# Kernel tuning notes

Hardware: AMD Instinct MI355X
Metric: run time of the kernel (lower is better)

The kernel has to match this reference:

```python
import jax, jax.numpy as jnp
import numpy as np

E_NODES_C = 50000   # constraints
E_NODES_V = 100000  # variables
N_EDGES = 1600000
EMB = 64
EDGE_NFEATS = 1
N_LAYERS = 2
N_CONVS = 2 * N_LAYERS  # v_to_c and c_to_v per layer
EPS = 1e-5


def setup_inputs() -> dict:
    key = jax.random.key(0)
    ks = jax.random.split(key, 24)
    s = 1.0 / np.sqrt(EMB)
    inp = {
        "constraint_features": jax.random.normal(ks[0], (E_NODES_C, EMB), jnp.float32),
        "variable_features": jax.random.normal(ks[1], (E_NODES_V, EMB), jnp.float32),
        "edge_indices": jnp.stack([
            jax.random.randint(ks[2], (N_EDGES,), 0, E_NODES_C, jnp.int32),
            jax.random.randint(ks[3], (N_EDGES,), 0, E_NODES_V, jnp.int32),
        ]),
        "edge_features": jax.random.normal(ks[4], (N_EDGES, EDGE_NFEATS), jnp.float32),
        # stacked params for the 4 conv blocks
        "Wl": jax.random.normal(ks[5], (N_CONVS, EMB, EMB), jnp.float32) * s,
        "bl": jnp.zeros((N_CONVS, EMB), jnp.float32),
        "We": jax.random.normal(ks[6], (N_CONVS, EMB, EDGE_NFEATS), jnp.float32) * s,
        "Wr": jax.random.normal(ks[7], (N_CONVS, EMB, EMB), jnp.float32) * s,
        "g1": jnp.ones((N_CONVS, EMB), jnp.float32),
        "b1": jnp.zeros((N_CONVS, EMB), jnp.float32),
        "Wf": jax.random.normal(ks[8], (N_CONVS, EMB, EMB), jnp.float32) * s,
        "bf": jnp.zeros((N_CONVS, EMB), jnp.float32),
        "g2": jnp.ones((N_CONVS, EMB), jnp.float32),
        "b2": jnp.zeros((N_CONVS, EMB), jnp.float32),
        "Wo1": jax.random.normal(ks[9], (N_CONVS, EMB, 2 * EMB), jnp.float32) * s,
        "bo1": jnp.zeros((N_CONVS, EMB), jnp.float32),
        "Wo2": jax.random.normal(ks[10], (N_CONVS, EMB, EMB), jnp.float32) * s,
        "bo2": jnp.zeros((N_CONVS, EMB), jnp.float32),
    }
    return inp


def _layer_norm(x, g, b):
    m = jnp.mean(x, axis=-1, keepdims=True)
    v = jnp.mean(jnp.square(x - m), axis=-1, keepdims=True)
    return (x - m) * jax.lax.rsqrt(v + EPS) * g + b


def _conv(k, left, src, dst, ef, right, P):
    # message: Lin(right_i) + Lin_nobias(edge) + Lin_nobias(left_j)
    h = (right[dst] @ P["Wl"][k].T + P["bl"][k]
         + ef @ P["We"][k].T
         + left[src] @ P["Wr"][k].T)                       # [E, emb]
    h = jax.nn.relu(_layer_norm(h, P["g1"][k], P["b1"][k]))
    h = h @ P["Wf"][k].T + P["bf"][k]
    agg = jax.ops.segment_sum(h, dst, num_segments=right.shape[0])  # [N_right, emb]
    z = jnp.concatenate([_layer_norm(agg, P["g2"][k], P["b2"][k]), right], axis=-1)
    return jax.nn.relu(z @ P["Wo1"][k].T + P["bo1"][k]) @ P["Wo2"][k].T + P["bo2"][k]


def reference(constraint_features, variable_features, edge_indices, edge_features,
              Wl, bl, We, Wr, g1, b1, Wf, bf, g2, b2, Wo1, bo1, Wo2, bo2):
    P = dict(Wl=Wl, bl=bl, We=We, Wr=Wr, g1=g1, b1=b1, Wf=Wf, bf=bf,
             g2=g2, b2=b2, Wo1=Wo1, bo1=bo1, Wo2=Wo2, bo2=bo2)
    ci, vi = edge_indices[0], edge_indices[1]
    c, v = constraint_features, variable_features
    for i in range(N_LAYERS):
        # v_to_c: left=variables (src=vi), right=constraints (dst=ci)
        c = c + _conv(2 * i, v, vi, ci, edge_features, c, P)
        # c_to_v: left=constraints (src=ci), right=variables (dst=vi)
        v = v + _conv(2 * i + 1, c, ci, vi, edge_features, v, P)
    return (c, v)
```

## Files before the change

kernel.cpp:

```cpp
#include <hip/hip_runtime.h>

#define EMB   64
#define NCON  50000
#define NVAR  100000
#define NEDGE 1600000
#define EPSLN 1e-5f

#define PADEC (NEDGE + 15 * NCON)
#define PADEV (NEDGE + 15 * NVAR)

#define HCHUNK 12544
#define HSEG   32
#define HCHC   4
#define HCHV   8

typedef _Float16 half2_t __attribute__((ext_vector_type(2)));
typedef _Float16 f16x8  __attribute__((ext_vector_type(8)));
typedef float    f32x2  __attribute__((ext_vector_type(2)));
typedef float    f32x4  __attribute__((ext_vector_type(4)));

template <int CTRL, int RMASK>
__device__ __forceinline__ float dpp_add_f(float x) {
    int m = __builtin_amdgcn_update_dpp(0, __builtin_bit_cast(int, x), CTRL, RMASK, 0xf, true);
    return x + __builtin_bit_cast(float, m);
}
__device__ __forceinline__ float wtotal64(float x) {
    x = dpp_add_f<0x111, 0xf>(x);
    x = dpp_add_f<0x112, 0xf>(x);
    x = dpp_add_f<0x114, 0xf>(x);
    x = dpp_add_f<0x118, 0xf>(x);
    x = dpp_add_f<0x142, 0xa>(x);
    x = dpp_add_f<0x143, 0xc>(x);
    return __builtin_bit_cast(float, __builtin_amdgcn_readlane(__builtin_bit_cast(int, x), 63));
}
template <int CTRL, int RMASK>
__device__ __forceinline__ int dpp_add_i(int x) {
    return x + __builtin_amdgcn_update_dpp(0, x, CTRL, RMASK, 0xf, true);
}
__device__ __forceinline__ int wtotal64_i(int x) {
    x = dpp_add_i<0x111, 0xf>(x);
    x = dpp_add_i<0x112, 0xf>(x);
    x = dpp_add_i<0x114, 0xf>(x);
    x = dpp_add_i<0x118, 0xf>(x);
    x = dpp_add_i<0x142, 0xa>(x);
    x = dpp_add_i<0x143, 0xc>(x);
    return __builtin_amdgcn_readlane(x, 63);
}

__device__ __forceinline__ float dot2f(half2_t a, half2_t b, float c) {
    return __builtin_amdgcn_fdot2(a, b, c, false);
}

__device__ __forceinline__ half2_t hmax2(half2_t a, half2_t b) {
#if defined(__has_builtin) && __has_builtin(__builtin_elementwise_max)
    return __builtin_elementwise_max(a, b);
#else
    half2_t r;
    r.x = a.x > b.x ? a.x : b.x;
    r.y = a.y > b.y ? a.y : b.y;
    return r;
#endif
}

__device__ __forceinline__ float matvec_f16(const _Float16* __restrict__ buf,
                                            const half2_t* __restrict__ wh, float acc) {
    const float4* hp4 = (const float4*)buf;
    float a0 = acc, a1 = 0.0f, a2 = 0.0f, a3 = 0.0f;
#pragma unroll
    for (int j4 = 0; j4 < 8; ++j4) {
        float4 t = hp4[j4];
        a0 = dot2f(wh[4 * j4 + 0], __builtin_bit_cast(half2_t, t.x), a0);
        a1 = dot2f(wh[4 * j4 + 1], __builtin_bit_cast(half2_t, t.y), a1);
        a2 = dot2f(wh[4 * j4 + 2], __builtin_bit_cast(half2_t, t.z), a2);
        a3 = dot2f(wh[4 * j4 + 3], __builtin_bit_cast(half2_t, t.w), a3);
    }
    return (a0 + a1) + (a2 + a3);
}

__device__ __forceinline__ void load_w_f16(const float* __restrict__ W, int stride,
                                           int lane, half2_t* wh) {
#pragma unroll
    for (int j4 = 0; j4 < 16; ++j4) {
        float4 t = *(const float4*)(W + (size_t)lane * stride + j4 * 4);
        wh[2 * j4 + 0] = half2_t{(_Float16)t.x, (_Float16)t.y};
        wh[2 * j4 + 1] = half2_t{(_Float16)t.z, (_Float16)t.w};
    }
}

__device__ __forceinline__ f16x8 cvt8_f16(float4 u, float4 v) {
    f16x8 r;
    r[0] = (_Float16)u.x; r[1] = (_Float16)u.y; r[2] = (_Float16)u.z; r[3] = (_Float16)u.w;
    r[4] = (_Float16)v.x; r[5] = (_Float16)v.y; r[6] = (_Float16)v.z; r[7] = (_Float16)v.w;
    return r;
}


__global__ __launch_bounds__(256) void hist_part_kernel(
        const int* __restrict__ ci, const int* __restrict__ vi,
        int* __restrict__ partC, int* __restrict__ partV, int E) {
    __shared__ int lh[HCHUNK];
    const int seg  = blockIdx.x % HSEG;
    const int cg   = blockIdx.x / HSEG;
    const bool isC = cg < HCHC;
    const int chunk = isC ? cg : cg - HCHC;
    const int base  = chunk * HCHUNK;
    const int* __restrict__ dst = isC ? ci : vi;
    int* __restrict__ part = (isC ? partC : partV) + (size_t)(chunk * HSEG + seg) * HCHUNK;

    int4* l4 = (int4*)lh;
    for (int i = threadIdx.x; i < HCHUNK / 4; i += 256) l4[i] = make_int4(0, 0, 0, 0);
    __syncthreads();

    const int s0 = (int)((long long)seg * E / HSEG);
    const int s1 = (int)((long long)(seg + 1) * E / HSEG);
    const int nvec = (s1 - s0) >> 2;
    const int4* d4 = (const int4*)(dst + s0);
    for (int i = threadIdx.x; i < nvec; i += 256) {
        const int4 t = d4[i];
        const unsigned r0 = (unsigned)(t.x - base);
        const unsigned r1 = (unsigned)(t.y - base);
        const unsigned r2 = (unsigned)(t.z - base);
        const unsigned r3 = (unsigned)(t.w - base);
        if (r0 < (unsigned)HCHUNK) atomicAdd(&lh[r0], 1);
        if (r1 < (unsigned)HCHUNK) atomicAdd(&lh[r1], 1);
        if (r2 < (unsigned)HCHUNK) atomicAdd(&lh[r2], 1);
        if (r3 < (unsigned)HCHUNK) atomicAdd(&lh[r3], 1);
    }
    for (int i = s0 + (nvec << 2) + threadIdx.x; i < s1; i += 256) {
        const unsigned rel = (unsigned)(dst[i] - base);
        if (rel < (unsigned)HCHUNK) atomicAdd(&lh[rel], 1);
    }
    __syncthreads();
    int4* p4 = (int4*)part;
    for (int i = threadIdx.x; i < HCHUNK / 4; i += 256) p4[i] = l4[i];
}

__global__ __launch_bounds__(256) void hist_reduce_kernel(
        const int* __restrict__ partC, const int* __restrict__ partV,
        int* __restrict__ degC, int* __restrict__ degV) {
    int j = blockIdx.x * blockDim.x + threadIdx.x;
    const int tot = NCON + NVAR;
    for (; j < tot; j += gridDim.x * blockDim.x) {
        if (j < NCON) {
            const int chunk = j / HCHUNK, off = j - chunk * HCHUNK;
            const int* p = partC + (size_t)chunk * HSEG * HCHUNK + off;
            int s = 0;
#pragma unroll
            for (int t = 0; t < HSEG; ++t) s += p[(size_t)t * HCHUNK];
            degC[j] = s;
        } else {
            const int jj = j - NCON;
            const int chunk = jj / HCHUNK, off = jj - chunk * HCHUNK;
            const int* p = partV + (size_t)chunk * HSEG * HCHUNK + off;
            int s = 0;
#pragma unroll
            for (int t = 0; t < HSEG; ++t) s += p[(size_t)t * HCHUNK];
            degV[jj] = s;
        }
    }
}

__global__ __launch_bounds__(256) void hist2_kernel(
        const int* __restrict__ ci, const int* __restrict__ vi,
        int* __restrict__ degC, int* __restrict__ degV, int E) {
    int i = blockIdx.x * blockDim.x + threadIdx.x;
    for (; i < E; i += gridDim.x * blockDim.x) {
        atomicAdd(&degC[ci[i]], 1);
        atomicAdd(&degV[vi[i]], 1);
    }
}

template <bool PAD>
__global__ __launch_bounds__(256) void chunk_sum_kernel(const int* __restrict__ hist,
                                                        int* __restrict__ csum, int N) {
    __shared__ int wpart[4];
    const int base = blockIdx.x * 1024 + threadIdx.x * 4;
    int s = 0;
    if (base + 3 < N) {
        int4 t = *(const int4*)(hist + base);
        if (PAD) s = ((t.x+15)&~15) + ((t.y+15)&~15) + ((t.z+15)&~15) + ((t.w+15)&~15);
        else     s = t.x + t.y + t.z + t.w;
    } else {
#pragma unroll
        for (int j = 0; j < 4; ++j)
            if (base + j < N) { int v = hist[base + j]; s += PAD ? ((v+15)&~15) : v; }
    }
    s = wtotal64_i(s);
    if ((threadIdx.x & 63) == 0) wpart[threadIdx.x >> 6] = s;
    __syncthreads();
    if (threadIdx.x == 0) csum[blockIdx.x] = wpart[0] + wpart[1] + wpart[2] + wpart[3];
}

__global__ void chunk_offsets_kernel(const int* __restrict__ csum, int* __restrict__ coff,
                                     int* __restrict__ rowptr, int nchunk, int N) {
    const int lane = threadIdx.x;
    int carry = 0;
    for (int base = 0; base < nchunk; base += 64) {
        const int i = base + lane;
        int val = (i < nchunk) ? csum[i] : 0;
        int incl = val;
#pragma unroll
        for (int off = 1; off < 64; off <<= 1) {
            int t = __shfl_up(incl, off, 64);
            if (lane >= off) incl += t;
        }
        if (i < nchunk) coff[i] = incl - val + carry;
        carry += __shfl(incl, 63, 64);
    }
    if (lane == 0) rowptr[N] = carry;
}

template <bool PAD>
__global__ __launch_bounds__(256) void chunk_apply_kernel(
        const int* __restrict__ hist, const int* __restrict__ coff,
        int* __restrict__ rowptr, int* __restrict__ cursor, int N) {
    __shared__ int wpart[4];
    const int wv = threadIdx.x >> 6;
    const int lane = threadIdx.x & 63;
    const int base = blockIdx.x * 1024 + threadIdx.x * 4;
    int v0 = 0, v1 = 0, v2 = 0, v3 = 0;
    if (base + 3 < N) {
        int4 t = *(const int4*)(hist + base);
        v0 = t.x; v1 = t.y; v2 = t.z; v3 = t.w;
    } else {
        if (base + 0 < N) v0 = hist[base + 0];
        if (base + 1 < N) v1 = hist[base + 1];
        if (base + 2 < N) v2 = hist[base + 2];
        if (base + 3 < N) v3 = hist[base + 3];
    }
    if (PAD) { v0 = (v0+15)&~15; v1 = (v1+15)&~15; v2 = (v2+15)&~15; v3 = (v3+15)&~15; }
    const int s = v0 + v1 + v2 + v3;
    int incl = s;
#pragma unroll
    for (int off = 1; off < 64; off <<= 1) {
        int t = __shfl_up(incl, off, 64);
        if (lane >= off) incl += t;
    }
    if (lane == 63) wpart[wv] = incl;
    __syncthreads();
    int excl = coff[blockIdx.x] + incl - s;
    for (int w = 0; w < wv; ++w) excl += wpart[w];
    if (base + 0 < N) { rowptr[base + 0] = excl; cursor[base + 0] = excl; excl += v0; }
    if (base + 1 < N) { rowptr[base + 1] = excl; cursor[base + 1] = excl; excl += v1; }
    if (base + 2 < N) { rowptr[base + 2] = excl; cursor[base + 2] = excl; excl += v2; }
    if (base + 3 < N) { rowptr[base + 3] = excl; cursor[base + 3] = excl; excl += v3; }
}

template <int NDST>
__global__ __launch_bounds__(256) void scatter_dir_kernel(
        const int* __restrict__ dst, const int* __restrict__ src,
        const float* __restrict__ ef,
        int* __restrict__ cur, int2* __restrict__ ep, int E) {
    const int rep = blockIdx.x & 7;
    const int stride = (gridDim.x >> 3) * blockDim.x;
    int i = (blockIdx.x >> 3) * blockDim.x + threadIdx.x;
    for (; i < E; i += stride) {
        const int d = dst[i];
        const int b = (int)(((long long)d * 8) / NDST);
        if (b == rep) {
            const int slot = atomicAdd(&cur[d], 1);
            ep[slot] = make_int2(src[i], __float_as_int(ef[i]));
        }
    }
}


__global__ __launch_bounds__(256, 3) void lin2_kernel(
        const float* __restrict__ XR, const float* __restrict__ WR,
        const float* __restrict__ bR, _Float16* __restrict__ YR, int NR,
        const float* __restrict__ XL, const float* __restrict__ WL,
        _Float16* __restrict__ YL, int NL, int nbR) {
    const int wv   = threadIdx.x >> 6;
    const int lane = threadIdx.x & 63;
    const int col  = lane & 15;
    const int kgrp = lane >> 4;
    const bool isR = (int)blockIdx.x < nbR;
    const float* X = isR ? XR : XL;
    const float* W = isR ? WR : WL;
    _Float16* Y    = isR ? YR : YL;
    const int N    = isR ? NR : NL;
    const int b0   = isR ? 0 : nbR;
    const int nb   = isR ? nbR : (gridDim.x - nbR);

    f16x8 bf[4][2];
#pragma unroll
    for (int ct = 0; ct < 4; ++ct)
#pragma unroll
        for (int kc = 0; kc < 2; ++kc) {
            const float* wrow = W + (size_t)(ct * 16 + col) * EMB + kc * 32 + kgrp * 8;
            bf[ct][kc] = cvt8_f16(*(const float4*)wrow, *(const float4*)(wrow + 4));
        }
    float bias[4];
#pragma unroll
    for (int ct = 0; ct < 4; ++ct) bias[ct] = isR ? bR[ct * 16 + col] : 0.0f;

    const int ntile = (N + 15) >> 4;
    const int nW = nb * 4;
    for (int t = ((int)blockIdx.x - b0) * 4 + wv; t < ntile; t += nW) {
        const int n0 = t << 4;
        const int srow = min(n0 + col, N - 1);
        const float* xrow = X + (size_t)srow * EMB + kgrp * 8;
        const float4 x0 = *(const float4*)(xrow);
        const float4 x1 = *(const float4*)(xrow + 4);
        const float4 x2 = *(const float4*)(xrow + 32);
        const float4 x3 = *(const float4*)(xrow + 36);
        const f16x8 a0 = cvt8_f16(x0, x1);
        const f16x8 a1 = cvt8_f16(x2, x3);
        f32x4 acc[4];
#pragma unroll
        for (int ct = 0; ct < 4; ++ct) {
            acc[ct] = __builtin_amdgcn_mfma_f32_16x16x32_f16(
                a0, bf[ct][0], (f32x4){0.0f, 0.0f, 0.0f, 0.0f}, 0, 0, 0);
            acc[ct] = __builtin_amdgcn_mfma_f32_16x16x32_f16(
                a1, bf[ct][1], acc[ct], 0, 0, 0);
        }
#pragma unroll
        for (int r = 0; r < 4; ++r) {
            const int n = n0 + (kgrp << 2) + r;
            if (n < N) {
                _Float16* yrow = Y + (size_t)n * EMB + col;
#pragma unroll
                for (int ct = 0; ct < 4; ++ct)
                    yrow[ct * 16] = (_Float16)(acc[ct][r] + bias[ct]);
            }
        }
    }
}


__global__ __launch_bounds__(256, 4) void edge_abar_kernel(
        const int* __restrict__ rp16, const int* __restrict__ deg,
        const int2* __restrict__ ep,
        const _Float16* __restrict__ RL, const _Float16* __restrict__ LL,
        const float* __restrict__ We, const float* __restrict__ g1,
        const float* __restrict__ b1, _Float16* __restrict__ ABAR, int Nr) {
    __shared__ __align__(16) float tbuf[4][16][68];
    const int wv   = threadIdx.x >> 6;
    const int lane = threadIdx.x & 63;
    const int col  = lane & 15;
    const int quad = lane >> 4;
    const int kb   = quad * 8;

    half2_t weh[8], gkh[8], bkh[8];
#pragma unroll
    for (int j = 0; j < 4; ++j) {
        weh[j]     = half2_t{(_Float16)We[kb + 2*j],      (_Float16)We[kb + 2*j + 1]};
        weh[4 + j] = half2_t{(_Float16)We[kb + 32 + 2*j], (_Float16)We[kb + 32 + 2*j + 1]};
        gkh[j]     = half2_t{(_Float16)g1[kb + 2*j],      (_Float16)g1[kb + 2*j + 1]};
        gkh[4 + j] = half2_t{(_Float16)g1[kb + 32 + 2*j], (_Float16)g1[kb + 32 + 2*j + 1]};
        bkh[j]     = half2_t{(_Float16)b1[kb + 2*j],      (_Float16)b1[kb + 2*j + 1]};
        bkh[4 + j] = half2_t{(_Float16)b1[kb + 32 + 2*j], (_Float16)b1[kb + 32 + 2*j + 1]};
    }

    const int nW = gridDim.x * 4;
    int n = blockIdx.x * 4 + wv;
    int pg0 = rp16[n] >> 4;
    int pg1 = rp16[n + 1] >> 4;
    int pdn = deg[n];

    bool livN = false; float fN = 0.0f;
    f16x8 llaN = {}, llbN = {};
    auto issue_group = [&](int gbase, int cnt) {
        livN = col < cnt;
        int2 p = ep[(gbase << 4) + col];
        const int s2 = livN ? p.x : 0;
        fN = livN ? __int_as_float(p.y) : 0.0f;
        llaN = *(const f16x8*)(LL + (size_t)s2 * EMB + kb);
        llbN = *(const f16x8*)(LL + (size_t)s2 * EMB + kb + 32);
    };
    if (pg0 < pg1) issue_group(pg0, pdn);

    while (true) {
        const int g0 = pg0, g1e = pg1, dn = pdn;
        const int nn = n + nW;
        const bool hasNext = nn < Nr;
        if (hasNext) {
            pg0 = rp16[nn] >> 4;
            pg1 = rp16[nn + 1] >> 4;
            pdn = deg[nn];
        }

        half2_t rl2[8];
        *(f16x8*)&rl2[0] = *(const f16x8*)(RL + (size_t)n * EMB + kb);
        *(f16x8*)&rl2[4] = *(const f16x8*)(RL + (size_t)n * EMB + kb + 32);

        f32x2 acc2[8];
#pragma unroll
        for (int j = 0; j < 8; ++j) acc2[j] = f32x2{0.0f, 0.0f};

        bool didNext = false;
        for (int g = g0; g < g1e; ++g) {
            const bool liv = livN;
            const float f = fN;
            half2_t h2[8];
            *(f16x8*)&h2[0] = llaN;
            *(f16x8*)&h2[4] = llbN;
            if (g + 1 < g1e) {
                issue_group(g + 1, dn - ((g + 1 - g0) << 4));
            } else if (hasNext && pg0 < pg1) {
                issue_group(pg0, pdn);
                didNext = true;
            }
            const _Float16 fh = (_Float16)f;
            const half2_t f2 = half2_t{fh, fh};
            const half2_t one2 = half2_t{(_Float16)1.0f, (_Float16)1.0f};
            float ps = 0.0f, pq = 0.0f;
#pragma unroll
            for (int j = 0; j < 8; ++j) {
                h2[j] = (h2[j] + rl2[j]) + f2 * weh[j];
                ps = dot2f(h2[j], one2, ps);
                pq = dot2f(h2[j], h2[j], pq);
            }
            ps += __shfl_xor(ps, 16, 64); ps += __shfl_xor(ps, 32, 64);
            pq += __shfl_xor(pq, 16, 64); pq += __shfl_xor(pq, 32, 64);
            const float mean = ps * (1.0f / EMB);
            const float var  = pq * (1.0f / EMB) - mean * mean;
            const float rs   = rsqrtf(var + EPSLN);
            const _Float16 rsh = (_Float16)rs;
            const _Float16 mnh = (_Float16)mean;
            const half2_t rs2 = half2_t{rsh, rsh};
            const half2_t mn2 = half2_t{mnh, mnh};
            const half2_t z2  = half2_t{(_Float16)0.0f, (_Float16)0.0f};
            if (liv) {
#pragma unroll
                for (int j = 0; j < 8; ++j) {
                    const half2_t sc = gkh[j] * rs2;
                    half2_t a = (h2[j] - mn2) * sc + bkh[j];
                    a = hmax2(a, z2);
                    f32x2 cv; cv.x = (float)a.x; cv.y = (float)a.y;
                    acc2[j] += cv;
                }
            }
        }

        float* tb = &tbuf[wv][col][0];
        *(float4*)(tb + kb)      = make_float4(acc2[0].x, acc2[0].y, acc2[1].x, acc2[1].y);
        *(float4*)(tb + kb + 4)  = make_float4(acc2[2].x, acc2[2].y, acc2[3].x, acc2[3].y);
        *(float4*)(tb + kb + 32) = make_float4(acc2[4].x, acc2[4].y, acc2[5].x, acc2[5].y);
        *(float4*)(tb + kb + 36) = make_float4(acc2[6].x, acc2[6].y, acc2[7].x, acc2[7].y);
        float t0[16];
#pragma unroll
        for (int c2 = 0; c2 < 16; ++c2) t0[c2] = tbuf[wv][c2][lane];
        const float s01 = (t0[0] + t0[1]) + (t0[2] + t0[3]);
        const float s23 = (t0[4] + t0[5]) + (t0[6] + t0[7]);
        const float s45 = (t0[8] + t0[9]) + (t0[10] + t0[11]);
        const float s67 = (t0[12] + t0[13]) + (t0[14] + t0[15]);
        ABAR[(size_t)n * EMB + lane] = (_Float16)((s01 + s23) + (s45 + s67));

        if (!hasNext) break;
        if (!didNext && pg0 < pg1) issue_group(pg0, pdn);
        n = nn;
    }
}


__global__ __launch_bounds__(256, 4) void edge_csr_kernel(
        const int* __restrict__ rowptr, const int2* __restrict__ ep,
        const _Float16* __restrict__ RL, const _Float16* __restrict__ LL,
        const float* __restrict__ Wecol, const float* __restrict__ g1,
        const float* __restrict__ b1,
        _Float16* __restrict__ ABAR, int Nr) {
    const int lane = threadIdx.x & 63;
    const float we  = Wecol[lane];
    const float g   = g1[lane];
    const float bb  = b1[lane];
    const int nW = gridDim.x * 4;
    for (int n = blockIdx.x * 4 + (threadIdx.x >> 6); n < Nr; n += nW) {
        const int beg = rowptr[n];
        const int end = rowptr[n + 1];
        const float rl = (float)RL[(size_t)n * EMB + lane];
        float acc = 0.0f;
        for (int idx = beg; idx < end; ++idx) {
            const int2 p = ep[idx];
            const float f = __int_as_float(p.y);
            float h = rl + (float)LL[(size_t)p.x * EMB + lane] + f * we;
            const float s1 = wtotal64(h);
            const float s2 = wtotal64(h * h);
            const float m   = s1 * (1.0f / EMB);
            const float var = s2 * (1.0f / EMB) - m * m;
            acc += fmaxf((h - m) * rsqrtf(var + EPSLN) * g + bb, 0.0f);
        }
        ABAR[(size_t)n * EMB + lane] = (_Float16)acc;
    }
}


__global__ __launch_bounds__(256, 1) void out_kernel(
        const _Float16* __restrict__ ABAR, const int* __restrict__ deg,
        float* __restrict__ right,
        const float* __restrict__ g2, const float* __restrict__ b2,
        const float* __restrict__ Wf, const float* __restrict__ bfp,
        const float* __restrict__ Wo1, const float* __restrict__ Wo2,
        const float* __restrict__ bo1, const float* __restrict__ bo2, int N) {
    __shared__ __align__(16) _Float16 zt[4][16][72];
    __shared__ __align__(16) _Float16 ot[4][16][72];
    const int wv   = threadIdx.x >> 6;
    const int lane = threadIdx.x & 63;
    const int col  = lane & 15;
    const int kgrp = lane >> 4;

    f16x8 bF[4][2], b1a[4][2], b1b[4][2], b2f[4][2];
#pragma unroll
    for (int ct = 0; ct < 4; ++ct)
#pragma unroll
        for (int kc = 0; kc < 2; ++kc) {
            const int row = ct * 16 + col;
            const int ko  = kc * 32 + kgrp * 8;
            const float* wf = Wf  + (size_t)row * EMB + ko;
            const float* w1 = Wo1 + (size_t)row * 2 * EMB + ko;
            const float* w2 = Wo2 + (size_t)row * EMB + ko;
            bF[ct][kc]  = cvt8_f16(*(const float4*)wf, *(const float4*)(wf + 4));
            b1a[ct][kc] = cvt8_f16(*(const float4*)w1, *(const float4*)(w1 + 4));
            b1b[ct][kc] = cvt8_f16(*(const float4*)(w1 + EMB), *(const float4*)(w1 + EMB + 4));
            b2f[ct][kc] = cvt8_f16(*(const float4*)w2, *(const float4*)(w2 + 4));
        }
    float bfc[4], gc[4], bbc[4], bo1c[4], bo2c[4];
#pragma unroll
    for (int ct = 0; ct < 4; ++ct) {
        const int cd = ct * 16 + col;
        bfc[ct]  = bfp[cd];
        gc[ct]   = g2[cd];
        bbc[ct]  = b2[cd];
        bo1c[ct] = bo1[cd];
        bo2c[ct] = bo2[cd];
    }

    const int ntile = N >> 4;
    const int nW = gridDim.x * 4;
    for (int t = blockIdx.x * 4 + wv; t < ntile; t += nW) {
        const int n0 = t << 4;
        const _Float16* arow = ABAR + (size_t)(n0 + col) * EMB + kgrp * 8;
        const f16x8 aA0 = *(const f16x8*)(arow);
        const f16x8 aA1 = *(const f16x8*)(arow + 32);
        f32x4 acc[4];
#pragma unroll
        for (int ct = 0; ct < 4; ++ct) {
            acc[ct] = __builtin_amdgcn_mfma_f32_16x16x32_f16(
                aA0, bF[ct][0], (f32x4){0.0f, 0.0f, 0.0f, 0.0f}, 0, 0, 0);
            acc[ct] = __builtin_amdgcn_mfma_f32_16x16x32_f16(
                aA1, bF[ct][1], acc[ct], 0, 0, 0);
        }
        float dnr[4];
#pragma unroll
        for (int r = 0; r < 4; ++r) dnr[r] = (float)deg[n0 + (kgrp << 2) + r];
#pragma unroll
        for (int r = 0; r < 4; ++r) {
            float s1 = 0.0f, s2 = 0.0f;
#pragma unroll
            for (int ct = 0; ct < 4; ++ct) {
                const float a = acc[ct][r] + dnr[r] * bfc[ct];
                acc[ct][r] = a;
                s1 += a; s2 += a * a;
            }
            s1 += __shfl_xor(s1, 1, 64); s2 += __shfl_xor(s2, 1, 64);
            s1 += __shfl_xor(s1, 2, 64); s2 += __shfl_xor(s2, 2, 64);
            s1 += __shfl_xor(s1, 4, 64); s2 += __shfl_xor(s2, 4, 64);
            s1 += __shfl_xor(s1, 8, 64); s2 += __shfl_xor(s2, 8, 64);
            const float mean = s1 * (1.0f / EMB);
            const float var  = s2 * (1.0f / EMB) - mean * mean;
            const float rs   = rsqrtf(var + EPSLN);
            const int zr = (kgrp << 2) + r;
#pragma unroll
            for (int ct = 0; ct < 4; ++ct)
                zt[wv][zr][ct * 16 + col] =
                    (_Float16)((acc[ct][r] - mean) * rs * gc[ct] + bbc[ct]);
        }
        const _Float16* zrow = &zt[wv][col][kgrp * 8];
        const f16x8 zA0 = *(const f16x8*)(zrow);
        const f16x8 zA1 = *(const f16x8*)(zrow + 32);
        const float* rrow = right + (size_t)(n0 + col) * EMB + kgrp * 8;
        const f16x8 rA0 = cvt8_f16(*(const float4*)(rrow), *(const float4*)(rrow + 4));
        const f16x8 rA1 = cvt8_f16(*(const float4*)(rrow + 32), *(const float4*)(rrow + 36));
        f32x4 acc3[4];
#pragma unroll
        for (int ct = 0; ct < 4; ++ct) {
            acc3[ct] = __builtin_amdgcn_mfma_f32_16x16x32_f16(
                zA0, b1a[ct][0], (f32x4){0.0f, 0.0f, 0.0f, 0.0f}, 0, 0, 0);
            acc3[ct] = __builtin_amdgcn_mfma_f32_16x16x32_f16(
                zA1, b1a[ct][1], acc3[ct], 0, 0, 0);
            acc3[ct] = __builtin_amdgcn_mfma_f32_16x16x32_f16(
                rA0, b1b[ct][0], acc3[ct], 0, 0, 0);
            acc3[ct] = __builtin_amdgcn_mfma_f32_16x16x32_f16(
                rA1, b1b[ct][1], acc3[ct], 0, 0, 0);
        }
#pragma unroll
        for (int r = 0; r < 4; ++r) {
            const int orr = (kgrp << 2) + r;
#pragma unroll
            for (int ct = 0; ct < 4; ++ct)
                ot[wv][orr][ct * 16 + col] =
                    (_Float16)fmaxf(acc3[ct][r] + bo1c[ct], 0.0f);
        }
        const _Float16* orow = &ot[wv][col][kgrp * 8];
        const f16x8 oA0 = *(const f16x8*)(orow);
        const f16x8 oA1 = *(const f16x8*)(orow + 32);
        f32x4 acc4[4];
#pragma unroll
        for (int ct = 0; ct < 4; ++ct) {
            acc4[ct] = __builtin_amdgcn_mfma_f32_16x16x32_f16(
                oA0, b2f[ct][0], (f32x4){0.0f, 0.0f, 0.0f, 0.0f}, 0, 0, 0);
            acc4[ct] = __builtin_amdgcn_mfma_f32_16x16x32_f16(
                oA1, b2f[ct][1], acc4[ct], 0, 0, 0);
        }
#pragma unroll
        for (int r = 0; r < 4; ++r) {
            float* rr = right + (size_t)(n0 + (kgrp << 2) + r) * EMB + col;
#pragma unroll
            for (int ct = 0; ct < 4; ++ct)
                rr[ct * 16] += acc4[ct][r] + bo2c[ct];
        }
    }
}

extern "C" void kernel_launch(void* const* d_in, const int* in_sizes, int n_in,
                              void* d_out, int out_size, void* d_ws, size_t ws_size,
                              hipStream_t stream) {
    const float* cf  = (const float*)d_in[0];
    const float* vfp = (const float*)d_in[1];
    const int*   ei  = (const int*)d_in[2];
    const float* ef  = (const float*)d_in[3];
    const float* Wl  = (const float*)d_in[4];
    const float* bl  = (const float*)d_in[5];
    const float* We  = (const float*)d_in[6];
    const float* Wr  = (const float*)d_in[7];
    const float* g1  = (const float*)d_in[8];
    const float* b1  = (const float*)d_in[9];
    const float* Wf  = (const float*)d_in[10];
    const float* bfp = (const float*)d_in[11];
    const float* g2  = (const float*)d_in[12];
    const float* b2  = (const float*)d_in[13];
    const float* Wo1 = (const float*)d_in[14];
    const float* bo1 = (const float*)d_in[15];
    const float* Wo2 = (const float*)d_in[16];
    const float* bo2 = (const float*)d_in[17];

    float* c = (float*)d_out;
    float* v = c + (size_t)NCON * EMB;
    (void)hipMemcpyAsync(c, cf,  (size_t)NCON * EMB * sizeof(float), hipMemcpyDeviceToDevice, stream);
    (void)hipMemcpyAsync(v, vfp, (size_t)NVAR * EMB * sizeof(float), hipMemcpyDeviceToDevice, stream);

    float* wsf = (float*)d_ws;
    size_t off = 0;
    _Float16* AGG = (_Float16*)(wsf + off); off += (size_t)NVAR * EMB / 2;
    _Float16* RL  = (_Float16*)(wsf + off); off += (size_t)NVAR * EMB / 2;
    _Float16* LL  = (_Float16*)(wsf + off); off += (size_t)NVAR * EMB / 2;
    int* degC  = (int*)(wsf + off); off += NCON;
    int* degV  = (int*)(wsf + off); off += NVAR;
    int* rp16C = (int*)(wsf + off); off += NCON + 4;
    int* curC  = (int*)(wsf + off); off += NCON;
    int* rp16V = (int*)(wsf + off); off += NVAR + 4;
    int* curV  = (int*)(wsf + off); off += NVAR;
    int* csumC = (int*)(wsf + off); off += 128;
    int* coffC = (int*)(wsf + off); off += 128;
    int* csumV = (int*)(wsf + off); off += 128;
    int* coffV = (int*)(wsf + off); off += 128;
    size_t off_edges = off;
    int2* epC = (int2*)(wsf + off); off += (size_t)2 * PADEC;
    int2* epV = (int2*)(wsf + off); off += (size_t)2 * PADEV;
    const bool use_mfma = ws_size >= off * sizeof(float);
    int* partC = (int*)(wsf + off); off += (size_t)HCHC * HSEG * HCHUNK;
    int* partV = (int*)(wsf + off); off += (size_t)HCHV * HSEG * HCHUNK;
    const bool use_ldshist = use_mfma && ws_size >= off * sizeof(float);
    if (!use_mfma) {
        off = off_edges;
        epC = (int2*)(wsf + off); off += (size_t)2 * NEDGE;
        epV = (int2*)(wsf + off); off += (size_t)2 * NEDGE;
    }

    const int* ci = ei;
    const int* vi = ei + NEDGE;

    const dim3 blk(256);
    const int NB = 2048;
    const int NBL = 1536;
    const int nchC = (NCON + 1023) / 1024;
    const int nchV = (NVAR + 1023) / 1024;

    if (use_ldshist) {
        hist_part_kernel<<<(HCHC + HCHV) * HSEG, blk, 0, stream>>>(ci, vi, partC, partV, NEDGE);
        hist_reduce_kernel<<<640, blk, 0, stream>>>(partC, partV, degC, degV);
    } else {
        (void)hipMemsetAsync(degC, 0, NCON * sizeof(int), stream);
        (void)hipMemsetAsync(degV, 0, NVAR * sizeof(int), stream);
        hist2_kernel<<<1024, blk, 0, stream>>>(ci, vi, degC, degV, NEDGE);
    }
    if (use_mfma) {
        chunk_sum_kernel<true><<<nchC, blk, 0, stream>>>(degC, csumC, NCON);
        chunk_sum_kernel<true><<<nchV, blk, 0, stream>>>(degV, csumV, NVAR);
        chunk_offsets_kernel<<<1, 64, 0, stream>>>(csumC, coffC, rp16C, nchC, NCON);
        chunk_offsets_kernel<<<1, 64, 0, stream>>>(csumV, coffV, rp16V, nchV, NVAR);
        chunk_apply_kernel<true><<<nchC, blk, 0, stream>>>(degC, coffC, rp16C, curC, NCON);
        chunk_apply_kernel<true><<<nchV, blk, 0, stream>>>(degV, coffV, rp16V, curV, NVAR);
    } else {
        chunk_sum_kernel<false><<<nchC, blk, 0, stream>>>(degC, csumC, NCON);
        chunk_sum_kernel<false><<<nchV, blk, 0, stream>>>(degV, csumV, NVAR);
        chunk_offsets_kernel<<<1, 64, 0, stream>>>(csumC, coffC, rp16C, nchC, NCON);
        chunk_offsets_kernel<<<1, 64, 0, stream>>>(csumV, coffV, rp16V, nchV, NVAR);
        chunk_apply_kernel<false><<<nchC, blk, 0, stream>>>(degC, coffC, rp16C, curC, NCON);
        chunk_apply_kernel<false><<<nchV, blk, 0, stream>>>(degV, coffV, rp16V, curV, NVAR);
    }
    scatter_dir_kernel<NCON><<<2048, blk, 0, stream>>>(ci, vi, ef, curC, epC, NEDGE);
    scatter_dir_kernel<NVAR><<<2048, blk, 0, stream>>>(vi, ci, ef, curV, epV, NEDGE);

    for (int k = 0; k < 4; ++k) {
        const bool v2c = ((k & 1) == 0);
        float* right   = v2c ? c : v;
        float* left    = v2c ? v : c;
        const int Nr   = v2c ? NCON : NVAR;
        const int Nl   = v2c ? NVAR : NCON;
        const int nbR  = v2c ? NBL / 3 : 2 * NBL / 3;
        const int* degR = v2c ? degC : degV;

        lin2_kernel<<<NBL, blk, 0, stream>>>(
            right, Wl + (size_t)k * EMB * EMB, bl + (size_t)k * EMB, RL, Nr,
            left,  Wr + (size_t)k * EMB * EMB, LL, Nl, nbR);

        if (use_mfma) {
            edge_abar_kernel<<<NB, blk, 0, stream>>>(
                v2c ? rp16C : rp16V, degR, v2c ? epC : epV,
                RL, LL, We + (size_t)k * EMB,
                g1 + (size_t)k * EMB, b1 + (size_t)k * EMB,
                AGG, Nr);
        } else {
            edge_csr_kernel<<<NB, blk, 0, stream>>>(
                v2c ? rp16C : rp16V, v2c ? epC : epV,
                RL, LL, We + (size_t)k * EMB,
                g1 + (size_t)k * EMB, b1 + (size_t)k * EMB,
                AGG, Nr);
        }
        out_kernel<<<NB, blk, 0, stream>>>(AGG, degR, right,
                                           g2 + (size_t)k * EMB, b2 + (size_t)k * EMB,
                                           Wf + (size_t)k * EMB * EMB,
                                           bfp + (size_t)k * EMB,
                                           Wo1 + (size_t)k * EMB * 2 * EMB,
                                           Wo2 + (size_t)k * EMB * EMB,
                                           bo1 + (size_t)k * EMB, bo2 + (size_t)k * EMB,
                                           Nr);
    }
}
```

Before: 916.1 us.

## Replace global-atomic edge scatter with LDS-cursor partitioned scatter using per-segment offsets

Splits the degree histogram into 20 smaller chunks per side, so each block's range fits in LDS and more blocks run. The per-segment partial histograms are then turned into exclusive start offsets, and a new scatter kernel uses LDS atomics on those cursors instead of global atomics when building the CSR edge lists. Each block re-reads its whole segment of destination indices and keeps only the edges in its chunk, so the index array is read many times. In return, slot assignment moves from contended global atomics to shared-memory atomics.

```diff
diff --git a/kernel.cpp b/kernel.cpp
--- a/kernel.cpp
+++ b/kernel.cpp
@@ -9,10 +9,11 @@
 #define PADEC (NEDGE + 15 * NCON)
 #define PADEV (NEDGE + 15 * NVAR)
 
-#define HCHUNK 12544
-#define HSEG   32
-#define HCHC   4
-#define HCHV   8
+#define HSEG 32
+#define NCHC 20
+#define CHNC 2500
+#define NCHV 20
+#define CHNV 5000
 
 typedef _Float16 half2_t __attribute__((ext_vector_type(2)));
 typedef _Float16 f16x8  __attribute__((ext_vector_type(8)));
@@ -98,17 +99,18 @@
 __global__ __launch_bounds__(256) void hist_part_kernel(
         const int* __restrict__ ci, const int* __restrict__ vi,
         int* __restrict__ partC, int* __restrict__ partV, int E) {
-    __shared__ int lh[HCHUNK];
-    const int seg  = blockIdx.x % HSEG;
-    const int cg   = blockIdx.x / HSEG;
-    const bool isC = cg < HCHC;
-    const int chunk = isC ? cg : cg - HCHC;
-    const int base  = chunk * HCHUNK;
+    __shared__ int lh[CHNV];
+    const int cg  = blockIdx.x % (NCHC + NCHV);
+    const int seg = blockIdx.x / (NCHC + NCHV);
+    const bool isC = cg < NCHC;
+    const int chunk  = isC ? cg : cg - NCHC;
+    const int chunkN = isC ? CHNC : CHNV;
+    const int base   = chunk * chunkN;
     const int* __restrict__ dst = isC ? ci : vi;
-    int* __restrict__ part = (isC ? partC : partV) + (size_t)(chunk * HSEG + seg) * HCHUNK;
+    int* __restrict__ part = (isC ? partC : partV) + (size_t)(chunk * HSEG + seg) * chunkN;
 
     int4* l4 = (int4*)lh;
-    for (int i = threadIdx.x; i < HCHUNK / 4; i += 256) l4[i] = make_int4(0, 0, 0, 0);
+    for (int i = threadIdx.x; i < chunkN / 4; i += 256) l4[i] = make_int4(0, 0, 0, 0);
     __syncthreads();
 
     const int s0 = (int)((long long)seg * E / HSEG);
@@ -121,18 +123,18 @@
         const unsigned r1 = (unsigned)(t.y - base);
         const unsigned r2 = (unsigned)(t.z - base);
         const unsigned r3 = (unsigned)(t.w - base);
-        if (r0 < (unsigned)HCHUNK) atomicAdd(&lh[r0], 1);
-        if (r1 < (unsigned)HCHUNK) atomicAdd(&lh[r1], 1);
-        if (r2 < (unsigned)HCHUNK) atomicAdd(&lh[r2], 1);
-        if (r3 < (unsigned)HCHUNK) atomicAdd(&lh[r3], 1);
+        if (r0 < (unsigned)chunkN) atomicAdd(&lh[r0], 1);
+        if (r1 < (unsigned)chunkN) atomicAdd(&lh[r1], 1);
+        if (r2 < (unsigned)chunkN) atomicAdd(&lh[r2], 1);
+        if (r3 < (unsigned)chunkN) atomicAdd(&lh[r3], 1);
     }
     for (int i = s0 + (nvec << 2) + threadIdx.x; i < s1; i += 256) {
         const unsigned rel = (unsigned)(dst[i] - base);
-        if (rel < (unsigned)HCHUNK) atomicAdd(&lh[rel], 1);
+        if (rel < (unsigned)chunkN) atomicAdd(&lh[rel], 1);
     }
     __syncthreads();
     int4* p4 = (int4*)part;
-    for (int i = threadIdx.x; i < HCHUNK / 4; i += 256) p4[i] = l4[i];
+    for (int i = threadIdx.x; i < chunkN / 4; i += 256) p4[i] = l4[i];
 }
 
 __global__ __launch_bounds__(256) void hist_reduce_kernel(
@@ -142,20 +144,108 @@
     const int tot = NCON + NVAR;
     for (; j < tot; j += gridDim.x * blockDim.x) {
         if (j < NCON) {
-            const int chunk = j / HCHUNK, off = j - chunk * HCHUNK;
-            const int* p = partC + (size_t)chunk * HSEG * HCHUNK + off;
+            const int chunk = j / CHNC, off = j - chunk * CHNC;
+            const int* p = partC + (size_t)chunk * HSEG * CHNC + off;
             int s = 0;
 #pragma unroll
-            for (int t = 0; t < HSEG; ++t) s += p[(size_t)t * HCHUNK];
+            for (int t = 0; t < HSEG; ++t) s += p[(size_t)t * CHNC];
             degC[j] = s;
         } else {
             const int jj = j - NCON;
-            const int chunk = jj / HCHUNK, off = jj - chunk * HCHUNK;
-            const int* p = partV + (size_t)chunk * HSEG * HCHUNK + off;
+            const int chunk = jj / CHNV, off = jj - chunk * CHNV;
+            const int* p = partV + (size_t)chunk * HSEG * CHNV + off;
             int s = 0;
 #pragma unroll
-            for (int t = 0; t < HSEG; ++t) s += p[(size_t)t * HCHUNK];
+            for (int t = 0; t < HSEG; ++t) s += p[(size_t)t * CHNV];
             degV[jj] = s;
+        }
+    }
+}
+
+__global__ __launch_bounds__(256) void seg_offsets_kernel(
+        int* __restrict__ partC, int* __restrict__ partV,
+        const int* __restrict__ rp16C, const int* __restrict__ rp16V) {
+    int j = blockIdx.x * blockDim.x + threadIdx.x;
+    const int tot = NCON + NVAR;
+    for (; j < tot; j += gridDim.x * blockDim.x) {
+        if (j < NCON) {
+            const int chunk = j / CHNC, off = j - chunk * CHNC;
+            int* p = partC + (size_t)chunk * HSEG * CHNC + off;
+            int run = rp16C[j];
+#pragma unroll
+            for (int t = 0; t < HSEG; ++t) {
+                const int old = p[(size_t)t * CHNC];
+                p[(size_t)t * CHNC] = run;
+                run += old;
+            }
+        } else {
+            const int jj = j - NCON;
+            const int chunk = jj / CHNV, off = jj - chunk * CHNV;
+            int* p = partV + (size_t)chunk * HSEG * CHNV + off;
+            int run = rp16V[jj];
+#pragma unroll
+            for (int t = 0; t < HSEG; ++t) {
+                const int old = p[(size_t)t * CHNV];
+                p[(size_t)t * CHNV] = run;
+                run += old;
+            }
+        }
+    }
+}
+
+__global__ __launch_bounds__(256) void scatter_lds_kernel(
+        const int* __restrict__ ci, const int* __restrict__ vi,
+        const float* __restrict__ ef,
+        int* __restrict__ partC, int* __restrict__ partV,
+        int2* __restrict__ epC, int2* __restrict__ epV, int E) {
+    __shared__ int lcur[CHNV];
+    const int cg  = blockIdx.x % (NCHC + NCHV);
+    const int seg = blockIdx.x / (NCHC + NCHV);
+    const bool isC = cg < NCHC;
+    const int chunk  = isC ? cg : cg - NCHC;
+    const int chunkN = isC ? CHNC : CHNV;
+    const int base   = chunk * chunkN;
+    const int* __restrict__ dst = isC ? ci : vi;
+    const int* __restrict__ src = isC ? vi : ci;
+    int2* __restrict__ ep = isC ? epC : epV;
+    int* __restrict__ curs = (isC ? partC : partV) + (size_t)(chunk * HSEG + seg) * chunkN;
+
+    for (int i = threadIdx.x; i < chunkN; i += 256) lcur[i] = curs[i];
+    __syncthreads();
+
+    const int s0 = (int)((long long)seg * E / HSEG);
+    const int s1 = (int)((long long)(seg + 1) * E / HSEG);
+    const int nvec = (s1 - s0) >> 2;
+    const int4* d4 = (const int4*)(dst + s0);
+    for (int i = threadIdx.x; i < nvec; i += 256) {
+        const int4 t = d4[i];
+        const int e0 = s0 + (i << 2);
+        const unsigned r0 = (unsigned)(t.x - base);
+        const unsigned r1 = (unsigned)(t.y - base);
+        const unsigned r2 = (unsigned)(t.z - base);
+        const unsigned r3 = (unsigned)(t.w - base);
+        if (r0 < (unsigned)chunkN) {
+            const int slot = atomicAdd(&lcur[r0], 1);
+            ep[slot] = make_int2(src[e0 + 0], __float_as_int(ef[e0 + 0]));
+        }
+        if (r1 < (unsigned)chunkN) {
+            const int slot = atomicAdd(&lcur[r1], 1);
+            ep[slot] = make_int2(src[e0 + 1], __float_as_int(ef[e0 + 1]));
+        }
+        if (r2 < (unsigned)chunkN) {
+            const int slot = atomicAdd(&lcur[r2], 1);
+            ep[slot] = make_int2(src[e0 + 2], __float_as_int(ef[e0 + 2]));
+        }
+        if (r3 < (unsigned)chunkN) {
+            const int slot = atomicAdd(&lcur[r3], 1);
+            ep[slot] = make_int2(src[e0 + 3], __float_as_int(ef[e0 + 3]));
+        }
+    }
+    for (int i = s0 + (nvec << 2) + threadIdx.x; i < s1; i += 256) {
+        const unsigned rel = (unsigned)(dst[i] - base);
+        if (rel < (unsigned)chunkN) {
+            const int slot = atomicAdd(&lcur[rel], 1);
+            ep[slot] = make_int2(src[i], __float_as_int(ef[i]));
         }
     }
 }
@@ -658,8 +748,8 @@
     int2* epC = (int2*)(wsf + off); off += (size_t)2 * PADEC;
     int2* epV = (int2*)(wsf + off); off += (size_t)2 * PADEV;
     const bool use_mfma = ws_size >= off * sizeof(float);
-    int* partC = (int*)(wsf + off); off += (size_t)HCHC * HSEG * HCHUNK;
-    int* partV = (int*)(wsf + off); off += (size_t)HCHV * HSEG * HCHUNK;
+    int* partC = (int*)(wsf + off); off += (size_t)NCHC * HSEG * CHNC;
+    int* partV = (int*)(wsf + off); off += (size_t)NCHV * HSEG * CHNV;
     const bool use_ldshist = use_mfma && ws_size >= off * sizeof(float);
     if (!use_mfma) {
         off = off_edges;
@@ -675,9 +765,10 @@
     const int NBL = 1536;
     const int nchC = (NCON + 1023) / 1024;
     const int nchV = (NVAR + 1023) / 1024;
+    const int NGRP = NCHC + NCHV;
 
     if (use_ldshist) {
-        hist_part_kernel<<<(HCHC + HCHV) * HSEG, blk, 0, stream>>>(ci, vi, partC, partV, NEDGE);
+        hist_part_kernel<<<NGRP * HSEG, blk, 0, stream>>>(ci, vi, partC, partV, NEDGE);
         hist_reduce_kernel<<<640, blk, 0, stream>>>(partC, partV, degC, degV);
     } else {
         (void)hipMemsetAsync(degC, 0, NCON * sizeof(int), stream);
@@ -699,8 +790,14 @@
         chunk_apply_kernel<false><<<nchC, blk, 0, stream>>>(degC, coffC, rp16C, curC, NCON);
         chunk_apply_kernel<false><<<nchV, blk, 0, stream>>>(degV, coffV, rp16V, curV, NVAR);
     }
-    scatter_dir_kernel<NCON><<<2048, blk, 0, stream>>>(ci, vi, ef, curC, epC, NEDGE);
-    scatter_dir_kernel<NVAR><<<2048, blk, 0, stream>>>(vi, ci, ef, curV, epV, NEDGE);
+    if (use_ldshist) {
+        seg_offsets_kernel<<<640, blk, 0, stream>>>(partC, partV, rp16C, rp16V);
+        scatter_lds_kernel<<<NGRP * HSEG, blk, 0, stream>>>(
+            ci, vi, ef, partC, partV, epC, epV, NEDGE);
+    } else {
+        scatter_dir_kernel<NCON><<<2048, blk, 0, stream>>>(ci, vi, ef, curC, epC, NEDGE);
+        scatter_dir_kernel<NVAR><<<2048, blk, 0, stream>>>(vi, ci, ef, curV, epV, NEDGE);
+    }
 
     for (int k = 0; k < 4; ++k) {
         const bool v2c = ((k & 1) == 0);
```

New measurement: 907.4 us. Within noise of the previous version (-0.9%).
